# Kernel optimization log

Hardware: AMD Instinct MI355X
Metric: run time of the kernel (lower is better)

The kernel has to match this reference:

```python
import jax, jax.numpy as jnp
import numpy as np

# Dimensions (see shape_source): B=4, fine grid 8x8 windows of 16x16 tokens,
# pooled by 4x4 -> global grid 32x32 -> 2x2 windows of 16x16 tokens.
B, H, W, M, C, NH = 4, 8, 8, 16, 256, 8
HD = C // NH
GW = 2  # global window grid (2x2)


def _ln(x, g, b):
    m = x.mean(-1, keepdims=True)
    v = ((x - m) ** 2).mean(-1, keepdims=True)
    return (x - m) / jnp.sqrt(v + 1e-5) * g + b


def _posemb(x, w1, b1, w2):
    # RelativePositionEmbed: MLP(2 -> 512 -> C) over normalized 2D coords.
    N = x.shape[1]
    ctx = int(round(N ** 0.5))
    half = ctx // 2
    r = jnp.arange(ctx, dtype=x.dtype)
    grid = jnp.stack(jnp.meshgrid(r, r, indexing='ij'))  # [2, ctx, ctx]
    coords = ((grid - half) / half).reshape(2, -1).T     # [N, 2]
    return x + jax.nn.relu(coords @ w1 + b1) @ w2


def _mlp(x, w1, b1, w2, b2):
    return jax.nn.gelu(x @ w1 + b1, approximate=False) @ w2 + b2


def _sattn_block(x, ln1g, ln1b, wqkv, bqkv, wo, bo, ln2g, ln2b, mw1, mb1, mw2, mb2):
    # Pre-norm windowed MHSA + MLP (all2all self-attention inside each window).
    bn, N, _ = x.shape
    h = _ln(x, ln1g, ln1b)
    q, k, v = jnp.split(h @ wqkv + bqkv, 3, axis=-1)
    q = q.reshape(bn, N, NH, HD)
    k = k.reshape(bn, N, NH, HD)
    v = v.reshape(bn, N, NH, HD)
    att = jax.nn.softmax(jnp.einsum('bnhd,bmhd->bhnm', q, k) / (HD ** 0.5), axis=-1)
    o = jnp.einsum('bhnm,bmhd->bnhd', att, v).reshape(bn, N, C)
    x = x + o @ wo + bo
    return x + _mlp(_ln(x, ln2g, ln2b), mw1, mb1, mw2, mb2)


def _forward(scale0, scale1, pe_w1, pe_b1, pe_w2, ln1_g, ln1_b, wqkv, bqkv,
             wo, bo, ln2_g, ln2_b, mlp_w1, mlp_b1, mlp_w2, mlp_b2):
    # 1) per-scale relative position embeddings (weight_share=False path)
    x0 = _posemb(scale0, pe_w1[0], pe_b1[0], pe_w2[0])  # [B*64, 256, C]
    x1 = _posemb(scale1, pe_w1[1], pe_b1[1], pe_w2[1])  # [B*4, 256, C]

    # 2) propagate_bottom_up: max-pool each 16x16 window by 4 -> 4x4,
    p = x0.reshape(B * H * W, 4, 4, 4, 4, C).max(axis=(2, 4))  # (r1,p1,r2,p2)->max over p
    p = p.reshape(B, H, W, 4, 4, C).transpose(0, 1, 3, 2, 4, 5).reshape(B, H * 4, W * 4, C)
    l2g = p.reshape(B, GW, M, GW, M, C).transpose(0, 1, 3, 2, 4, 5).reshape(B * GW * GW, M * M, C)
    x1 = x1 + l2g

    # 3) all2all self-attention per scale (coarse to fine order; independent)
    o1 = _sattn_block(x1, ln1_g[1], ln1_b[1], wqkv[1], bqkv[1], wo[1], bo[1],
                      ln2_g[1], ln2_b[1], mlp_w1[1], mlp_b1[1], mlp_w2[1], mlp_b2[1])
    o0 = _sattn_block(x0, ln1_g[0], ln1_b[0], wqkv[0], bqkv[0], wo[0], bo[0],
                      ln2_g[0], ln2_b[0], mlp_w1[0], mlp_b1[0], mlp_w2[0], mlp_b2[0])

    # 4) one2one cross-attention aggregation: each global token queries the
    #    4x4 fine-token region it was pooled from (one-to-one mapping).
    fine = o0.reshape(B, H, W, 4, 4, 4, 4, C).transpose(0, 1, 2, 3, 5, 4, 6, 7)
    fine = fine.reshape(B * H * W * 16, 16, C)  # [B*1024, 16, C], order (b,h,w,r1,r2)
    g = o1.reshape(B, GW, GW, M, M, C).transpose(0, 1, 3, 2, 4, 5).reshape(B, 32, 32, C)
    g = g.reshape(B, H, 4, W, 4, C).transpose(0, 1, 3, 2, 4, 5).reshape(B * H * W * 16, 1, C)

    qn = _ln(g, ln1_g[1], ln1_b[1])
    kn = _ln(fine, ln1_g[1], ln1_b[1])
    wq, wk, wv = jnp.split(wqkv[1], 3, axis=-1)
    bq, bk, bv = jnp.split(bqkv[1], 3)
    q = (qn @ wq + bq).reshape(-1, 1, NH, HD)
    k = (kn @ wk + bk).reshape(-1, 16, NH, HD)
    v = (kn @ wv + bv).reshape(-1, 16, NH, HD)
    att = jax.nn.softmax(jnp.einsum('bnhd,bmhd->bhnm', q, k) / (HD ** 0.5), axis=-1)
    o = jnp.einsum('bhnm,bmhd->bnhd', att, v).reshape(-1, 1, C)
    g = g + o @ wo[1] + bo[1]
    g = g + _mlp(_ln(g, ln2_g[1], ln2_b[1]), mlp_w1[1], mlp_b1[1], mlp_w2[1], mlp_b2[1])

    # back to global window layout [B*4, 256, C]
    g = g.reshape(B, H, W, 4, 4, C).transpose(0, 1, 3, 2, 4, 5).reshape(B, 32, 32, C)
    o1 = g.reshape(B, GW, M, GW, M, C).transpose(0, 1, 3, 2, 4, 5).reshape(B * GW * GW, M * M, C)

    # concat on window axis so the harness sees a single output array
    return jnp.concatenate([o0, o1], axis=0)  # [272, 256, C]


def setup_inputs() -> dict:
    key = jax.random.key(0)
    ks = jax.random.split(key, 8)

    def w(k, shape):
        return jax.random.normal(k, shape, jnp.float32) * 0.02

    return {
        'scale0': jax.random.normal(ks[0], (B * H * W, M * M, C), jnp.float32),
        'scale1': jax.random.normal(ks[1], (B * GW * GW, M * M, C), jnp.float32),
        'pe_w1': w(ks[2], (2, 2, 512)), 'pe_b1': jnp.zeros((2, 512), jnp.float32),
        'pe_w2': w(ks[3], (2, 512, C)),
        'ln1_g': jnp.ones((2, C), jnp.float32), 'ln1_b': jnp.zeros((2, C), jnp.float32),
        'wqkv': w(ks[4], (2, C, 3 * C)), 'bqkv': jnp.zeros((2, 3 * C), jnp.float32),
        'wo': w(ks[5], (2, C, C)), 'bo': jnp.zeros((2, C), jnp.float32),
        'ln2_g': jnp.ones((2, C), jnp.float32), 'ln2_b': jnp.zeros((2, C), jnp.float32),
        'mlp_w1': w(ks[6], (2, C, 4 * C)), 'mlp_b1': jnp.zeros((2, 4 * C), jnp.float32),
        'mlp_w2': w(ks[7], (2, 4 * C, C)), 'mlp_b2': jnp.zeros((2, C), jnp.float32),
    }


def reference(scale0, scale1, pe_w1, pe_b1, pe_w2, ln1_g, ln1_b, wqkv, bqkv,
              wo, bo, ln2_g, ln2_b, mlp_w1, mlp_b1, mlp_w2, mlp_b2):
    return _forward(scale0, scale1, pe_w1, pe_b1, pe_w2, ln1_g, ln1_b, wqkv,
                    bqkv, wo, bo, ln2_g, ln2_b, mlp_w1, mlp_b1, mlp_w2, mlp_b2)
```

## Files before the change

kernel.cpp:

```cpp
#include <hip/hip_runtime.h>
#include <hip/hip_bf16.h>
#include <hip/hip_fp16.h>

#define ROWS0 65536
#define ROWS1 4096

typedef _Float16 half8 __attribute__((ext_vector_type(8)));
typedef _Float16 half4_t __attribute__((ext_vector_type(4)));
typedef float floatx4 __attribute__((ext_vector_type(4)));

#define LDSP(p) ((__attribute__((address_space(3))) void*)(p))
#define GLBP(p) ((const __attribute__((address_space(1))) void*)(p))

__device__ __forceinline__ float gelu_f(float x) {
    return 0.5f * x * (1.0f + erff(x * 0.70710678118654752f));
}

__global__ __launch_bounds__(256) void pe_kernel(
    const float* __restrict__ w1, const float* __restrict__ b1,
    const float* __restrict__ w2, float* __restrict__ pe)
{
    __shared__ float hid[512];
    int blk = blockIdx.x;
    int s = blk >> 8, n = blk & 255;
    int i = n >> 4, j = n & 15;
    float c0 = (i - 8) * 0.125f;
    float c1 = (j - 8) * 0.125f;
    int t = threadIdx.x;
    for (int hh = t; hh < 512; hh += 256) {
        float hv = c0 * w1[s * 1024 + hh] + c1 * w1[s * 1024 + 512 + hh] + b1[s * 512 + hh];
        hid[hh] = fmaxf(hv, 0.f);
    }
    __syncthreads();
    float o = 0.f;
    const float* w2p = w2 + (size_t)s * 512 * 256 + t;
    #pragma unroll 8
    for (int hh = 0; hh < 512; hh++) o += hid[hh] * w2p[hh * 256];
    pe[(size_t)s * 65536 + n * 256 + t] = o;
}

__global__ __launch_bounds__(256) void add_pe0_kernel(
    const float* __restrict__ s0, const float* __restrict__ pe, float* __restrict__ out)
{
    int row = blockIdx.x, c = threadIdx.x;
    out[(size_t)row * 256 + c] = s0[(size_t)row * 256 + c] + pe[(row & 255) * 256 + c];
}

__global__ __launch_bounds__(256) void pool_kernel(
    const float* __restrict__ x0, const float* __restrict__ s1,
    const float* __restrict__ pe1, float* __restrict__ x1out)
{
    int w1 = blockIdx.x >> 8, n1 = blockIdx.x & 255, c = threadIdx.x;
    int b = w1 >> 2, wy = (w1 >> 1) & 1, wx = w1 & 1;
    int ty = n1 >> 4, tx = n1 & 15;
    int gy = wy * 16 + ty, gx = wx * 16 + tx;
    int h = gy >> 2, r1 = gy & 3, w = gx >> 2, r2 = gx & 3;
    int fw = (b * 8 + h) * 8 + w;
    const float* base = x0 + ((size_t)fw * 256 + r1 * 64 + r2 * 4) * 256 + c;
    float mv = -1e30f;
    #pragma unroll
    for (int p1 = 0; p1 < 4; p1++)
        #pragma unroll
        for (int p2 = 0; p2 < 4; p2++)
            mv = fmaxf(mv, base[(p1 * 16 + p2) * 256]);
    size_t oidx = ((size_t)w1 * 256 + n1) * 256 + c;
    x1out[oidx] = s1[oidx] + pe1[n1 * 256 + c] + mv;
}

__global__ __launch_bounds__(256) void ln16_kernel(
    const float* __restrict__ X, const float* __restrict__ g,
    const float* __restrict__ b, _Float16* __restrict__ Y)
{
    __shared__ float smr[4];
    int row = blockIdx.x, t = threadIdx.x;
    float x = X[(size_t)row * 256 + t];
    float v = x;
    for (int o = 32; o; o >>= 1) v += __shfl_down(v, o);
    if ((t & 63) == 0) smr[t >> 6] = v;
    __syncthreads();
    float mean = (smr[0] + smr[1] + smr[2] + smr[3]) * (1.0f / 256.0f);
    __syncthreads();
    float d = x - mean;
    float vv = d * d;
    for (int o = 32; o; o >>= 1) vv += __shfl_down(vv, o);
    if ((t & 63) == 0) smr[t >> 6] = vv;
    __syncthreads();
    float var = (smr[0] + smr[1] + smr[2] + smr[3]) * (1.0f / 256.0f);
    float inv = 1.0f / sqrtf(var + 1e-5f);
    Y[(size_t)row * 256 + t] = (_Float16)(d * inv * g[t] + b[t]);
}

__global__ __launch_bounds__(256) void transposeW_kernel(
    const float* __restrict__ src, _Float16* __restrict__ dst, int K, int N)
{
    __shared__ float t[32][33];
    int k0 = blockIdx.y * 32, n0 = blockIdx.x * 32;
    int tx = threadIdx.x & 31, ty = threadIdx.x >> 5;
    for (int r = ty; r < 32; r += 8) t[r][tx] = src[(size_t)(k0 + r) * N + n0 + tx];
    __syncthreads();
    for (int r = ty; r < 32; r += 8) dst[(size_t)(n0 + r) * K + k0 + tx] = (_Float16)t[tx][r];
}

template<int ACT, int RES, int OUT16>
__global__ __launch_bounds__(256) void hgemm_kernel(
    const _Float16* __restrict__ A, const _Float16* __restrict__ Bw,
    const float* __restrict__ bias, const float* __restrict__ Res,
    void* __restrict__ Yv, int M, int N, int K)
{
    __shared__ alignas(16) _Float16 As[128 * 64];
    __shared__ alignas(16) _Float16 Bs[128 * 64];
    int tid = threadIdx.x;
    int m0 = blockIdx.y << 7, n0 = blockIdx.x << 7;
    int wave = tid >> 6, lane = tid & 63;
    int wr = wave >> 1, wc = wave & 1;
    floatx4 acc[4][4] = {};

    for (int k0 = 0; k0 < K; k0 += 64) {
        #pragma unroll
        for (int p = 0; p < 4; p++) {
            int s = tid + (p << 8);
            int row = s >> 3, phys = s & 7;
            int logc = phys ^ (row & 7);
            const _Float16* ga = A + (size_t)(m0 + row) * K + k0 + logc * 8;
            __builtin_amdgcn_global_load_lds(GLBP(ga), LDSP(&As[s * 8]), 16, 0, 0);
            const _Float16* gb = Bw + (size_t)(n0 + row) * K + k0 + logc * 8;
            __builtin_amdgcn_global_load_lds(GLBP(gb), LDSP(&Bs[s * 8]), 16, 0, 0);
        }
        __syncthreads();
        int r = lane & 15, c = lane >> 4;
        #pragma unroll
        for (int ks = 0; ks < 2; ks++) {
            half8 af[4], bf[4];
            #pragma unroll
            for (int i = 0; i < 4; i++) {
                int ra = wr * 64 + i * 16 + r;
                af[i] = *(const half8*)&As[ra * 64 + (((ks << 2) | c) ^ (ra & 7)) * 8];
                int rb = wc * 64 + i * 16 + r;
                bf[i] = *(const half8*)&Bs[rb * 64 + (((ks << 2) | c) ^ (rb & 7)) * 8];
            }
            #pragma unroll
            for (int i = 0; i < 4; i++)
                #pragma unroll
                for (int j = 0; j < 4; j++)
                    acc[i][j] = __builtin_amdgcn_mfma_f32_16x16x32_f16(af[i], bf[j], acc[i][j], 0, 0, 0);
        }
        __syncthreads();
    }

    int r = lane & 15, qrow = lane >> 4;
    #pragma unroll
    for (int j = 0; j < 4; j++) {
        int col = n0 + wc * 64 + j * 16 + r;
        float bj = bias[col];
        #pragma unroll
        for (int i = 0; i < 4; i++) {
            int rowb = m0 + wr * 64 + i * 16 + qrow * 4;
            #pragma unroll
            for (int reg = 0; reg < 4; reg++) {
                int row = rowb + reg;
                float v = acc[i][j][reg] + bj;
                if (ACT) v = gelu_f(v);
                if (RES) v += Res[(size_t)row * N + col];
                if (OUT16) ((_Float16*)Yv)[(size_t)row * N + col] = (_Float16)v;
                else       ((float*)Yv)[(size_t)row * N + col] = v;
            }
        }
    }
}

__global__ __launch_bounds__(256) void attn_mfma_kernel(
    const _Float16* __restrict__ qkv, _Float16* __restrict__ out)
{
    __shared__ alignas(16) _Float16 Klds[8192];
    __shared__ alignas(16) _Float16 Qlds[8192];
    __shared__ alignas(16) _Float16 VT[8192];
    __shared__ alignas(16) _Float16 Pl[4][4096];

    int tid = threadIdx.x;
    int win = blockIdx.x, head = blockIdx.y;
    int w = tid >> 6, lane = tid & 63;
    int r = lane & 15, h = lane >> 4;

    {
        const _Float16* base = qkv + ((size_t)(win * 256 + tid)) * 768 + head * 32;
        half8 qv[4], kv[4], vv[4];
        #pragma unroll
        for (int c = 0; c < 4; c++) {
            qv[c] = *(const half8*)(base + c * 8);
            kv[c] = *(const half8*)(base + 256 + c * 8);
            vv[c] = *(const half8*)(base + 512 + c * 8);
        }
        int rowbase = (tid >> 1) * 64;
        #pragma unroll
        for (int c = 0; c < 4; c++) {
            int phys = (((tid & 1) << 2) + c) ^ ((tid >> 1) & 7);
            *(half8*)&Qlds[rowbase + phys * 8] = qv[c];
            *(half8*)&Klds[rowbase + phys * 8] = kv[c];
        }
        #pragma unroll
        for (int d = 0; d < 32; d++)
            VT[d * 256 + (((tid >> 3) ^ (d & 7)) << 3) + (tid & 7)] = vv[d >> 3][d & 7];
    }
    __syncthreads();

    half8 vf[2][8];
    #pragma unroll
    for (int dc = 0; dc < 2; dc++)
        #pragma unroll
        for (int kc2 = 0; kc2 < 8; kc2++)
            vf[dc][kc2] = *(const half8*)&VT[(dc * 16 + r) * 256 + ((((kc2 << 2) + h) ^ (r & 7)) << 3)];

    const floatx4 zf = {0.f, 0.f, 0.f, 0.f};
    int physa = (((r & 1) << 2) + h) ^ ((r >> 1) & 7);

    for (int g = 0; g < 4; g++) {
        int qg = (w << 2) + g;
        half8 qb = *(const half8*)&Qlds[((qg << 3) + (r >> 1)) * 64 + physa * 8];
        floatx4 s[16];
        #pragma unroll
        for (int kc = 0; kc < 16; kc++) {
            half8 ka = *(const half8*)&Klds[((kc << 3) + (r >> 1)) * 64 + physa * 8];
            s[kc] = __builtin_amdgcn_mfma_f32_16x16x32_f16(ka, qb, zf, 0, 0, 0);
        }
        float m = -1e30f;
        #pragma unroll
        for (int kc = 0; kc < 16; kc++)
            #pragma unroll
            for (int e = 0; e < 4; e++) m = fmaxf(m, s[kc][e]);
        m = fmaxf(m, __shfl_xor(m, 16));
        m = fmaxf(m, __shfl_xor(m, 32));
        float l = 0.f;
        #pragma unroll
        for (int kc = 0; kc < 16; kc++)
            #pragma unroll
            for (int e = 0; e < 4; e++) {
                float p = __expf((s[kc][e] - m) * 0.17677669529663687f);
                s[kc][e] = p;
                l += p;
            }
        l += __shfl_xor(l, 16);
        l += __shfl_xor(l, 32);
        float inv = 1.0f / l;
        #pragma unroll
        for (int kc = 0; kc < 16; kc++) {
            half4_t pk;
            pk[0] = (_Float16)s[kc][0]; pk[1] = (_Float16)s[kc][1];
            pk[2] = (_Float16)s[kc][2]; pk[3] = (_Float16)s[kc][3];
            *(half4_t*)&Pl[w][r * 256 + ((((kc << 1) + (h >> 1)) ^ (r & 7)) << 3) + ((h & 1) << 2)] = pk;
        }
        floatx4 o0 = zf, o1 = zf;
        #pragma unroll
        for (int kc2 = 0; kc2 < 8; kc2++) {
            half8 pb = *(const half8*)&Pl[w][r * 256 + ((((kc2 << 2) + h) ^ (r & 7)) << 3)];
            o0 = __builtin_amdgcn_mfma_f32_16x16x32_f16(vf[0][kc2], pb, o0, 0, 0, 0);
            o1 = __builtin_amdgcn_mfma_f32_16x16x32_f16(vf[1][kc2], pb, o1, 0, 0, 0);
        }
        #pragma unroll
        for (int dc = 0; dc < 2; dc++) {
            floatx4 o = dc ? o1 : o0;
            half4_t oh;
            #pragma unroll
            for (int e = 0; e < 4; e++) oh[e] = (_Float16)(o[e] * inv);
            *(half4_t*)&Pl[w][(r >> 1) * 64 + (((((r & 1) << 2) + (dc << 1) + (h >> 1)) ^ ((r >> 1) & 7)) << 3) + ((h & 1) << 2)] = oh;
        }
        int q2 = lane >> 2, c2 = lane & 3;
        half8 ov = *(const half8*)&Pl[w][(q2 >> 1) * 64 + (((((q2 & 1) << 2) + c2) ^ ((q2 >> 1) & 7)) << 3)];
        *(half8*)(out + ((size_t)(win * 256 + qg * 16 + q2)) * 256 + head * 32 + c2 * 8) = ov;
    }
}

__global__ __launch_bounds__(128) void cross_attn_kernel(
    const _Float16* __restrict__ Qb, const _Float16* __restrict__ KV,
    _Float16* __restrict__ Ob, int fw0)
{
    __shared__ float att_s[8][16];
    int t = threadIdx.x;
    int lw = blockIdx.x >> 4;
    int sub = blockIdx.x & 15;
    int r1 = sub >> 2, r2 = sub & 3;
    int gi = (fw0 + lw) * 16 + sub;
    int h = t >> 4, m = t & 15;
    int p1 = m >> 2, p2 = m & 3;
    int lr = lw * 256 + r1 * 64 + p1 * 16 + r2 * 4 + p2;
    const half8* qp = (const half8*)(Qb + (size_t)gi * 256 + h * 32);
    const half8* kp = (const half8*)(KV + (size_t)lr * 512 + h * 32);
    float sc = 0.f;
    #pragma unroll
    for (int d8 = 0; d8 < 4; d8++) {
        half8 qv = qp[d8], kv = kp[d8];
        #pragma unroll
        for (int j = 0; j < 8; j++) sc += (float)qv[j] * (float)kv[j];
    }
    sc *= 0.17677669529663687f;
    float mx = sc;
    for (int o = 8; o; o >>= 1) mx = fmaxf(mx, __shfl_xor(mx, o));
    float e = __expf(sc - mx);
    float ssum = e;
    for (int o = 8; o; o >>= 1) ssum += __shfl_xor(ssum, o);
    att_s[h][m] = e / ssum;
    __syncthreads();
    int dg = t & 15;
    int d0 = dg * 2;
    float o0 = 0.f, o1 = 0.f;
    #pragma unroll
    for (int mm = 0; mm < 16; mm++) {
        int pp1 = mm >> 2, pp2 = mm & 3;
        int lrr = lw * 256 + r1 * 64 + pp1 * 16 + r2 * 4 + pp2;
        const _Float16* vp = KV + (size_t)lrr * 512 + 256 + h * 32;
        float a = att_s[h][mm];
        o0 += a * (float)vp[d0];
        o1 += a * (float)vp[d0 + 1];
    }
    Ob[(size_t)gi * 256 + h * 32 + d0]     = (_Float16)o0;
    Ob[(size_t)gi * 256 + h * 32 + d0 + 1] = (_Float16)o1;
}

__global__ __launch_bounds__(256) void gather_g_kernel(
    const float* __restrict__ o1, float* __restrict__ G)
{
    int gi = blockIdx.x, c = threadIdx.x;
    int b = gi >> 10, rem = gi & 1023;
    int h = rem >> 7, w = (rem >> 4) & 7, r1 = (rem >> 2) & 3, r2 = rem & 3;
    int gy = h * 4 + r1, gx = w * 4 + r2;
    int w1 = (b * 2 + (gy >> 4)) * 2 + (gx >> 4);
    int n1 = (gy & 15) * 16 + (gx & 15);
    G[(size_t)gi * 256 + c] = o1[((size_t)w1 * 256 + n1) * 256 + c];
}

__global__ __launch_bounds__(256) void scatter_g_kernel(
    const float* __restrict__ G, float* __restrict__ o1)
{
    int gi = blockIdx.x, c = threadIdx.x;
    int b = gi >> 10, rem = gi & 1023;
    int h = rem >> 7, w = (rem >> 4) & 7, r1 = (rem >> 2) & 3, r2 = rem & 3;
    int gy = h * 4 + r1, gx = w * 4 + r2;
    int w1 = (b * 2 + (gy >> 4)) * 2 + (gx >> 4);
    int n1 = (gy & 15) * 16 + (gx & 15);
    o1[((size_t)w1 * 256 + n1) * 256 + c] = G[(size_t)gi * 256 + c];
}

extern "C" void kernel_launch(void* const* d_in, const int* in_sizes, int n_in,
                              void* d_out, int out_size, void* d_ws, size_t ws_size,
                              hipStream_t stream)
{
    const float* scale0 = (const float*)d_in[0];
    const float* scale1 = (const float*)d_in[1];
    const float* pe_w1  = (const float*)d_in[2];
    const float* pe_b1  = (const float*)d_in[3];
    const float* pe_w2  = (const float*)d_in[4];
    const float* ln1_g  = (const float*)d_in[5];
    const float* ln1_b  = (const float*)d_in[6];
    const float* wqkv   = (const float*)d_in[7];
    const float* bqkv   = (const float*)d_in[8];
    const float* wo     = (const float*)d_in[9];
    const float* bo     = (const float*)d_in[10];
    const float* ln2_g  = (const float*)d_in[11];
    const float* ln2_b  = (const float*)d_in[12];
    const float* mw1    = (const float*)d_in[13];
    const float* mb1    = (const float*)d_in[14];
    const float* mw2    = (const float*)d_in[15];
    const float* mb2    = (const float*)d_in[16];
    float* out = (float*)d_out;
    char* arena = (char*)d_ws;

    float*    PE     = (float*)arena;              arena += 131072 * 4;
    float*    G      = (float*)arena;              arena += (size_t)4096 * 256 * 4;
    _Float16* Q16    = (_Float16*)arena;           arena += (size_t)4096 * 256 * 2;
    _Float16* OX16   = (_Float16*)arena;           arena += (size_t)4096 * 256 * 2;
    _Float16* wqkvT  = (_Float16*)arena;           arena += (size_t)2 * 768 * 256 * 2;
    _Float16* woT    = (_Float16*)arena;           arena += (size_t)2 * 256 * 256 * 2;
    _Float16* mw1T   = (_Float16*)arena;           arena += (size_t)2 * 1024 * 256 * 2;
    _Float16* mw2T   = (_Float16*)arena;           arena += (size_t)2 * 256 * 1024 * 2;
    size_t fixed_bytes = (size_t)(arena - (char*)d_ws);

    int R = 8192;
    if (fixed_bytes + (size_t)65536 * 4608 <= ws_size) R = 65536;
    else if (fixed_bytes + (size_t)32768 * 4608 <= ws_size) R = 32768;
    else if (fixed_bytes + (size_t)16384 * 4608 <= ws_size) R = 16384;
    int NC = 65536 / R;
    int CW = R / 256;

    _Float16* bufH16 = (_Float16*)arena;           arena += (size_t)R * 256 * 2;
    _Float16* qkv16  = (_Float16*)arena;           arena += (size_t)R * 768 * 2;
    _Float16* hid16  = (_Float16*)arena;           arena += (size_t)R * 1024 * 2;
    _Float16* o16    = (_Float16*)arena;

    auto hgemm = [&](const _Float16* A, const _Float16* Bw, const float* bias,
                     const float* Res, void* Y, int M, int N, int K, int act) {
        dim3 g(N >> 7, M >> 7);
        if (act)           hgemm_kernel<1, 0, 1><<<g, 256, 0, stream>>>(A, Bw, bias, nullptr, Y, M, N, K);
        else if (Res)      hgemm_kernel<0, 1, 0><<<g, 256, 0, stream>>>(A, Bw, bias, Res, Y, M, N, K);
        else               hgemm_kernel<0, 0, 1><<<g, 256, 0, stream>>>(A, Bw, bias, nullptr, Y, M, N, K);
    };

    auto sattn = [&](float* x, int Mrows, int nw, int s) {
        ln16_kernel<<<Mrows, 256, 0, stream>>>(x, ln1_g + s * 256, ln1_b + s * 256, bufH16);
        hgemm(bufH16, wqkvT + (size_t)s * 196608, bqkv + s * 768, nullptr, qkv16, Mrows, 768, 256, 0);
        attn_mfma_kernel<<<dim3(nw, 8), 256, 0, stream>>>(qkv16, o16);
        hgemm(o16, woT + (size_t)s * 65536, bo + s * 256, x, x, Mrows, 256, 256, 0);
        ln16_kernel<<<Mrows, 256, 0, stream>>>(x, ln2_g + s * 256, ln2_b + s * 256, bufH16);
        hgemm(bufH16, mw1T + (size_t)s * 262144, mb1 + s * 1024, nullptr, hid16, Mrows, 1024, 256, 1);
        hgemm(hid16, mw2T + (size_t)s * 262144, mb2 + s * 256, x, x, Mrows, 256, 1024, 0);
    };

    float* o1sec = out + (size_t)ROWS0 * 256;

    transposeW_kernel<<<dim3(768 / 32, 256 / 32), 256, 0, stream>>>(wqkv, wqkvT, 256, 768);
    transposeW_kernel<<<dim3(768 / 32, 256 / 32), 256, 0, stream>>>(wqkv + 196608, wqkvT + 196608, 256, 768);
    transposeW_kernel<<<dim3(256 / 32, 256 / 32), 256, 0, stream>>>(wo, woT, 256, 256);
    transposeW_kernel<<<dim3(256 / 32, 256 / 32), 256, 0, stream>>>(wo + 65536, woT + 65536, 256, 256);
    transposeW_kernel<<<dim3(1024 / 32, 256 / 32), 256, 0, stream>>>(mw1, mw1T, 256, 1024);
    transposeW_kernel<<<dim3(1024 / 32, 256 / 32), 256, 0, stream>>>(mw1 + 262144, mw1T + 262144, 256, 1024);
    transposeW_kernel<<<dim3(256 / 32, 1024 / 32), 256, 0, stream>>>(mw2, mw2T, 1024, 256);
    transposeW_kernel<<<dim3(256 / 32, 1024 / 32), 256, 0, stream>>>(mw2 + 262144, mw2T + 262144, 1024, 256);

    pe_kernel<<<512, 256, 0, stream>>>(pe_w1, pe_b1, pe_w2, PE);
    add_pe0_kernel<<<ROWS0, 256, 0, stream>>>(scale0, PE, out);
    pool_kernel<<<ROWS1, 256, 0, stream>>>(out, scale1, PE + 65536, o1sec);

    sattn(o1sec, ROWS1, 16, 1);
    for (int c = 0; c < NC; c++)
        sattn(out + (size_t)c * R * 256, R, CW, 0);

    gather_g_kernel<<<4096, 256, 0, stream>>>(o1sec, G);
    ln16_kernel<<<4096, 256, 0, stream>>>(G, ln1_g + 256, ln1_b + 256, bufH16);
    hgemm(bufH16, wqkvT + 196608, bqkv + 768, nullptr, Q16, 4096, 256, 256, 0);
    for (int c = 0; c < NC; c++) {
        float* xch = out + (size_t)c * R * 256;
        ln16_kernel<<<R, 256, 0, stream>>>(xch, ln1_g + 256, ln1_b + 256, bufH16);
        hgemm(bufH16, wqkvT + 196608 + 65536, bqkv + 768 + 256, nullptr, qkv16, R, 512, 256, 0);
        cross_attn_kernel<<<CW * 16, 128, 0, stream>>>(Q16, qkv16, OX16, c * CW);
    }
    hgemm(OX16, woT + 65536, bo + 256, G, G, 4096, 256, 256, 0);
    ln16_kernel<<<4096, 256, 0, stream>>>(G, ln2_g + 256, ln2_b + 256, bufH16);
    hgemm(bufH16, mw1T + 262144, mb1 + 1024, nullptr, hid16, 4096, 1024, 256, 1);
    hgemm(hid16, mw2T + 262144, mb2 + 256, G, G, 4096, 256, 1024, 0);
    scatter_g_kernel<<<4096, 256, 0, stream>>>(G, o1sec);
}
```

Baseline: 937.9 us.

## Stage GEMM epilogue through LDS for vectorized stores and remap workgroups per XCD

The GEMM epilogue now writes each wave's 16x64 output tile into shared memory and then issues 16-byte vectorized global stores (and vectorized residual loads) instead of scattered scalar stores. The launch switches to a 1D grid, and block ids are remapped so consecutive tiles land on the same XCD under MI355X's round-robin dispatch, improving L2 reuse of A/B tiles. The remap assumes the workgroup count is divisible by 8, and the epilogue reuses the operand LDS, which is safe only because of the trailing __syncthreads in the k-loop.

After: 914.6 us. 1.03x faster.

```diff
diff --git a/kernel.cpp b/kernel.cpp
--- a/kernel.cpp
+++ b/kernel.cpp
@@ -107,10 +107,17 @@
     const float* __restrict__ bias, const float* __restrict__ Res,
     void* __restrict__ Yv, int M, int N, int K)
 {
-    __shared__ alignas(16) _Float16 As[128 * 64];
-    __shared__ alignas(16) _Float16 Bs[128 * 64];
+    __shared__ alignas(16) _Float16 smem[2 * 128 * 64];
+    _Float16* As = smem;
+    _Float16* Bs = smem + 8192;
     int tid = threadIdx.x;
-    int m0 = blockIdx.y << 7, n0 = blockIdx.x << 7;
+
+    int gx = N >> 7;
+    int nwg = gx * (M >> 7);
+    int q8 = nwg >> 3;
+    int wg = (blockIdx.x & 7) * q8 + (blockIdx.x >> 3);
+    int m0 = (wg / gx) << 7, n0 = (wg % gx) << 7;
+
     int wave = tid >> 6, lane = tid & 63;
     int wr = wave >> 1, wc = wave & 1;
     floatx4 acc[4][4] = {};
@@ -148,21 +155,53 @@
     }
 
     int r = lane & 15, qrow = lane >> 4;
-    #pragma unroll
-    for (int j = 0; j < 4; j++) {
-        int col = n0 + wc * 64 + j * 16 + r;
-        float bj = bias[col];
+    if (OUT16) {
+        _Float16* sth = smem + wave * 1024;
         #pragma unroll
         for (int i = 0; i < 4; i++) {
-            int rowb = m0 + wr * 64 + i * 16 + qrow * 4;
-            #pragma unroll
-            for (int reg = 0; reg < 4; reg++) {
-                int row = rowb + reg;
-                float v = acc[i][j][reg] + bj;
-                if (ACT) v = gelu_f(v);
-                if (RES) v += Res[(size_t)row * N + col];
-                if (OUT16) ((_Float16*)Yv)[(size_t)row * N + col] = (_Float16)v;
-                else       ((float*)Yv)[(size_t)row * N + col] = v;
+            #pragma unroll
+            for (int j = 0; j < 4; j++) {
+                float bj = bias[n0 + wc * 64 + j * 16 + r];
+                #pragma unroll
+                for (int reg = 0; reg < 4; reg++) {
+                    float v = acc[i][j][reg] + bj;
+                    if (ACT) v = gelu_f(v);
+                    sth[(qrow * 4 + reg) * 64 + j * 16 + r] = (_Float16)v;
+                }
+            }
+            #pragma unroll
+            for (int p = 0; p < 2; p++) {
+                int row = p * 8 + (lane >> 3);
+                half8 hv = *(const half8*)&sth[row * 64 + (lane & 7) * 8];
+                *(half8*)((_Float16*)Yv + (size_t)(m0 + wr * 64 + i * 16 + row) * N
+                          + n0 + wc * 64 + (lane & 7) * 8) = hv;
+            }
+        }
+    } else {
+        float* stf = (float*)smem + wave * 1024;
+        #pragma unroll
+        for (int i = 0; i < 4; i++) {
+            #pragma unroll
+            for (int j = 0; j < 4; j++) {
+                float bj = bias[n0 + wc * 64 + j * 16 + r];
+                #pragma unroll
+                for (int reg = 0; reg < 4; reg++) {
+                    float v = acc[i][j][reg] + bj;
+                    if (ACT) v = gelu_f(v);
+                    stf[(qrow * 4 + reg) * 64 + j * 16 + r] = v;
+                }
+            }
+            #pragma unroll
+            for (int p = 0; p < 4; p++) {
+                int row = p * 4 + (lane >> 4);
+                float4 fv = *(const float4*)&stf[row * 64 + (lane & 15) * 4];
+                size_t ga = (size_t)(m0 + wr * 64 + i * 16 + row) * N
+                            + n0 + wc * 64 + (lane & 15) * 4;
+                if (RES) {
+                    float4 rv = *(const float4*)(Res + ga);
+                    fv.x += rv.x; fv.y += rv.y; fv.z += rv.z; fv.w += rv.w;
+                }
+                *(float4*)((float*)Yv + ga) = fv;
             }
         }
     }
@@ -387,10 +426,10 @@
 
     auto hgemm = [&](const _Float16* A, const _Float16* Bw, const float* bias,
                      const float* Res, void* Y, int M, int N, int K, int act) {
-        dim3 g(N >> 7, M >> 7);
-        if (act)           hgemm_kernel<1, 0, 1><<<g, 256, 0, stream>>>(A, Bw, bias, nullptr, Y, M, N, K);
-        else if (Res)      hgemm_kernel<0, 1, 0><<<g, 256, 0, stream>>>(A, Bw, bias, Res, Y, M, N, K);
-        else               hgemm_kernel<0, 0, 1><<<g, 256, 0, stream>>>(A, Bw, bias, nullptr, Y, M, N, K);
+        int nwg = (N >> 7) * (M >> 7);
+        if (act)           hgemm_kernel<1, 0, 1><<<nwg, 256, 0, stream>>>(A, Bw, bias, nullptr, Y, M, N, K);
+        else if (Res)      hgemm_kernel<0, 1, 0><<<nwg, 256, 0, stream>>>(A, Bw, bias, Res, Y, M, N, K);
+        else               hgemm_kernel<0, 0, 1><<<nwg, 256, 0, stream>>>(A, Bw, bias, nullptr, Y, M, N, K);
     };
 
     auto sattn = [&](float* x, int Mrows, int nw, int s) {
```
